# Kernel optimization log

Hardware: AMD Instinct MI355X
Metric: run time of the kernel (lower is better)

## Reference

```python
import jax, jax.numpy as jnp
import numpy as np

ALPHA = 0.01
EPS = ALPHA / (1.0 - 2.0 * ALPHA)  # boundary_eps


def setup_inputs() -> dict:
    key = jax.random.key(0)
    ks = jax.random.split(key, 9)
    B, D, K = 32768, 256, 1024
    x = jax.random.normal(ks[0], (B, D), dtype=jnp.float32)
    logp = jnp.zeros((B, 1), dtype=jnp.float32)
    actnorm1_bias = jax.random.normal(ks[1], (D,), dtype=jnp.float32) * 0.1
    actnorm1_weight = jax.random.normal(ks[2], (D,), dtype=jnp.float32) * 0.1
    actnorm2_bias = jax.random.normal(ks[3], (D,), dtype=jnp.float32) * 0.1
    actnorm2_weight = jax.random.normal(ks[4], (D,), dtype=jnp.float32) * 0.1
    shift_coeff = jax.random.normal(ks[5], (D,), dtype=jnp.float32)
    anchor_pts = jax.random.normal(ks[6], (K, D), dtype=jnp.float32)
    mixture_logits = jax.random.normal(ks[7], (K,), dtype=jnp.float32) * 0.1
    u = jax.random.uniform(ks[8], (D,), dtype=jnp.float32)
    box_min = -(u + 1.0) * 2.0  # guarantees box_max > box_min
    box_max = (u + 1.0) * 2.0
    return dict(x=x, logp=logp, actnorm1_bias=actnorm1_bias,
                actnorm1_weight=actnorm1_weight, actnorm2_bias=actnorm2_bias,
                actnorm2_weight=actnorm2_weight, shift_coeff=shift_coeff,
                anchor_pts=anchor_pts, mixture_logits=mixture_logits,
                box_min=box_min, box_max=box_max)


def _voronoi_forward(x, logp, a1b, a1w, a2b, a2w, shift_raw, anchors, mix_logits,
                     box_min, box_max):
    B, D = x.shape
    # actnorm1: y = (x + bias) * exp(weight); logp -= logdet
    x = (x + a1b) * jnp.exp(a1w)
    logp = logp - jnp.sum(a1w)
    # logit_transform.inverse: x = (sigmoid(x) - alpha) / (1 - 2*alpha)
    s = jax.nn.sigmoid(x)
    logdet = jnp.sum(jax.nn.log_sigmoid(x) + jax.nn.log_sigmoid(-x)
                     - jnp.log(1.0 - 2.0 * ALPHA), axis=1, keepdims=True)
    x = (s - ALPHA) / (1.0 - 2.0 * ALPHA)
    logp = logp - logdet
    # rescale from [-eps, 1+eps] to [0, 1]
    lo, hi = -EPS, 1.0 + EPS
    x = (x - lo) / (hi - lo)
    logp = logp - (-jnp.log(hi - lo) * D)
    # box constraints: affine to [box_min, box_max]
    x = x * (box_max - box_min) + box_min
    logp = logp - jnp.sum(jnp.log(box_max - box_min))
    # find_nearest: argmin squared distance over K anchors (GEMM form, no BxKxD tensor)
    d2 = (jnp.sum(x * x, axis=1, keepdims=True)
          - 2.0 * x @ anchors.T
          + jnp.sum(anchors * anchors, axis=1))  # [B, K]
    idx = jnp.argmin(d2, axis=1)  # [B]
    x_k = anchors[idx]  # gather nearest anchor, [B, D]
    # shift toward the nearest anchor
    sc = jax.nn.sigmoid(shift_raw) * 0.98 + 0.01  # (0.01, 0.99)
    x = x + sc * (x_k - x)
    logp = logp - jnp.sum(jnp.log(1.0 - sc))
    # map_outside_cell: identity with zero logdet (see notes)
    # recentre on the chosen anchor
    x = x - x_k
    # actnorm2
    x = (x + a2b) * jnp.exp(a2w)
    logp = logp - jnp.sum(a2w)
    # mixture log-prob gather
    logp_k = jax.nn.log_softmax(mix_logits)[idx][:, None]
    logp = logp - logp_k
    return x, logp, idx


def reference(x, logp, actnorm1_bias, actnorm1_weight, actnorm2_bias,
              actnorm2_weight, shift_coeff, anchor_pts, mixture_logits,
              box_min, box_max):
    return _voronoi_forward(x, logp, actnorm1_bias, actnorm1_weight,
                            actnorm2_bias, actnorm2_weight, shift_coeff,
                            anchor_pts, mixture_logits, box_min, box_max)
```

## Files before the change

### kernel.cpp

```cpp
#include <hip/hip_runtime.h>
#include <math.h>

namespace {
constexpr int Brows = 32768;
constexpr int Dd = 256;
constexpr int Kk = 1024;

constexpr double kAlpha64 = 0.01;
constexpr double kC164 = 1.0 - 2.0 * 0.01;
constexpr double kEps64 = 0.01 / (1.0 - 2.0 * 0.01);
constexpr double kLo64 = -kEps64;
constexpr double kHi64 = 1.0 + kEps64;

constexpr int WS_E1W = 0;
constexpr int WS_WD = 256;
constexpr int WS_P = 512;
constexpr int WS_Q = 768;
constexpr int WS_C = 1024;
constexpr int WS_AA = 1088;
constexpr int WS_LSM = 2112;
}

__global__ void precol_kernel(const float* __restrict__ a1w,
                              const float* __restrict__ a2w,
                              const float* __restrict__ a2b,
                              const float* __restrict__ shiftc,
                              const float* __restrict__ bmin,
                              const float* __restrict__ bmax,
                              float* __restrict__ ws) {
  const int d = threadIdx.x;
  const float w1 = a1w[d], w2 = a2w[d];
  const float wd = __fsub_rn(bmax[d], bmin[d]);
  const float sc = 1.0f / (1.0f + expf(-shiftc[d])) * 0.98f + 0.01f;
  const float e2 = expf(w2);
  ws[WS_E1W + d] = expf(w1);
  ws[WS_WD + d] = wd;
  ws[WS_P + d] = (1.0f - sc) * e2;
  ws[WS_Q + d] = a2b[d] * e2;
  float contrib = -w1 - w2 - logf(wd) - logf(1.0f - sc);
#pragma unroll
  for (int o = 32; o > 0; o >>= 1) contrib += __shfl_xor(contrib, o, 64);
  __shared__ float red[4];
  if ((d & 63) == 0) red[d >> 6] = contrib;
  __syncthreads();
  if (d == 0) {
    float Cv = red[0] + red[1] + red[2] + red[3];
    Cv += (float)Dd * (float)(log(kC164) + log(kHi64 - kLo64));
    ws[WS_C] = Cv;
  }
}

template <typename F>
__device__ inline float pw128_sq(F ld) {
  float r[8];
#pragma unroll
  for (int j = 0; j < 8; ++j) {
    const float v = ld(j);
    r[j] = __fmul_rn(v, v);
  }
  for (int i = 8; i < 128; i += 8) {
#pragma unroll
    for (int j = 0; j < 8; ++j) {
      const float v = ld(i + j);
      r[j] = __fadd_rn(r[j], __fmul_rn(v, v));
    }
  }
  const float s01 = __fadd_rn(r[0], r[1]);
  const float s23 = __fadd_rn(r[2], r[3]);
  const float s45 = __fadd_rn(r[4], r[5]);
  const float s67 = __fadd_rn(r[6], r[7]);
  return __fadd_rn(__fadd_rn(s01, s23), __fadd_rn(s45, s67));
}

__global__ void anorm_kernel(const float* __restrict__ anchors,
                             float* __restrict__ ws) {
  const int k = blockIdx.x * 256 + threadIdx.x;
  const float* a = anchors + (size_t)k * Dd;
  const float b0 = pw128_sq([&](int i) { return a[i]; });
  const float b1 = pw128_sq([&](int i) { return a[128 + i]; });
  ws[WS_AA + k] = __fadd_rn(b0, b1);
}

__global__ void lsm_kernel(const float* __restrict__ logits,
                           float* __restrict__ ws) {
  __shared__ float sm[1024];
  const int t = threadIdx.x;
  const float v = logits[t];
  sm[t] = v;
  __syncthreads();
  for (int o = 512; o > 0; o >>= 1) {
    if (t < o) sm[t] = fmaxf(sm[t], sm[t + o]);
    __syncthreads();
  }
  const float mx = sm[0];
  __syncthreads();
  sm[t] = expf(v - mx);
  __syncthreads();
  for (int o = 512; o > 0; o >>= 1) {
    if (t < o) sm[t] += sm[t + o];
    __syncthreads();
  }
  const float lse = mx + logf(sm[0]);
  ws[WS_LSM + t] = v - lse;
}

__global__ __launch_bounds__(256, 2) void voronoi_main(
    const float* __restrict__ x, const float* __restrict__ logp_in,
    const float* __restrict__ a1b, const float* __restrict__ anchors,
    const float* __restrict__ bmin, const float* __restrict__ ws,
    float* __restrict__ out) {
  __shared__ float xt[Dd][68];
  __shared__ float at[32][68];
  __shared__ float logdet_s[64];
  __shared__ float xx_s[64];
  __shared__ int bidx_s[64];

  const int t = threadIdx.x;
  const int r0 = blockIdx.x * 64;

  const float LOF = (float)kLo64;
  const float HLF = (float)(kHi64 - kLo64);
  const float ALPHAF = (float)kAlpha64;
  const float C1F = (float)kC164;

  {
    const int r = t >> 2, j = t & 3;
    const float* xrow = x + (size_t)(r0 + r) * Dd;
    float ld = 0.0f;
#pragma unroll
    for (int it = 0; it < 16; ++it) {
      const int c = it * 16 + j * 4;
      const float4 xv = *(const float4*)(xrow + c);
      const float4 bv = *(const float4*)(a1b + c);
      const float4 ev = *(const float4*)(ws + WS_E1W + c);
      const float4 wv = *(const float4*)(ws + WS_WD + c);
      const float4 mv = *(const float4*)(bmin + c);
      const float xs[4] = {xv.x, xv.y, xv.z, xv.w};
      const float bs[4] = {bv.x, bv.y, bv.z, bv.w};
      const float es[4] = {ev.x, ev.y, ev.z, ev.w};
      const float wds[4] = {wv.x, wv.y, wv.z, wv.w};
      const float ms[4] = {mv.x, mv.y, mv.z, mv.w};
#pragma unroll
      for (int w = 0; w < 4; ++w) {
        const float y = __fmul_rn(__fadd_rn(xs[w], bs[w]), es[w]);
        const float ay = fabsf(y);
        const float e = expf(-ay);
        ld += -ay - 2.0f * log1pf(e);
        const float den = __fadd_rn(1.0f, e);
        const float s =
            (y >= 0.0f) ? __fdiv_rn(1.0f, den) : __fdiv_rn(e, den);
        const float x3 = __fdiv_rn(__fsub_rn(s, ALPHAF), C1F);
        const float x4v = __fdiv_rn(__fsub_rn(x3, LOF), HLF);
        const float x5 = __fadd_rn(__fmul_rn(x4v, wds[w]), ms[w]);
        xt[c + w][r] = x5;
      }
    }
    ld += __shfl_xor(ld, 1, 64);
    ld += __shfl_xor(ld, 2, 64);
    if (j == 0) logdet_s[r] = ld;
  }
  __syncthreads();

  if (t < 64) {
    const float b0 = pw128_sq([&](int i) { return xt[i][t]; });
    const float b1 = pw128_sq([&](int i) { return xt[128 + i][t]; });
    xx_s[t] = __fadd_rn(b0, b1);
  }
  __syncthreads();

  const int tc = t & 15, tr = t >> 4;
  const int tr4 = tr * 4, tc4 = tc * 4;
  float xxr[4];
#pragma unroll
  for (int i = 0; i < 4; ++i) xxr[i] = xx_s[tr4 + i];
  float bd2[4];
  int bidx[4];
#pragma unroll
  for (int i = 0; i < 4; ++i) {
    bd2[i] = 3.0e38f;
    bidx[i] = 0;
  }

  for (int kt = 0; kt < 16; ++kt) {
    float acc[4][4];
#pragma unroll
    for (int i = 0; i < 4; ++i)
#pragma unroll
      for (int j = 0; j < 4; ++j) acc[i][j] = 0.0f;

    for (int dc = 0; dc < 8; ++dc) {
      __syncthreads();
#pragma unroll
      for (int m = 0; m < 2; ++m) {
        const int f = t + m * 256;
        const int kk = f >> 3, cp = f & 7;
        const float4 av = *(const float4*)(anchors +
                                           (size_t)(kt * 64 + kk) * Dd +
                                           dc * 32 + cp * 4);
        at[cp * 4 + 0][kk] = av.x;
        at[cp * 4 + 1][kk] = av.y;
        at[cp * 4 + 2][kk] = av.z;
        at[cp * 4 + 3][kk] = av.w;
      }
      __syncthreads();
      const int db = dc * 32;
#pragma unroll
      for (int dd = 0; dd < 32; ++dd) {
        const float4 xf = *(const float4*)(&xt[db + dd][tr4]);
        const float4 af = *(const float4*)(&at[dd][tc4]);
        acc[0][0] = fmaf(xf.x, af.x, acc[0][0]);
        acc[0][1] = fmaf(xf.x, af.y, acc[0][1]);
        acc[0][2] = fmaf(xf.x, af.z, acc[0][2]);
        acc[0][3] = fmaf(xf.x, af.w, acc[0][3]);
        acc[1][0] = fmaf(xf.y, af.x, acc[1][0]);
        acc[1][1] = fmaf(xf.y, af.y, acc[1][1]);
        acc[1][2] = fmaf(xf.y, af.z, acc[1][2]);
        acc[1][3] = fmaf(xf.y, af.w, acc[1][3]);
        acc[2][0] = fmaf(xf.z, af.x, acc[2][0]);
        acc[2][1] = fmaf(xf.z, af.y, acc[2][1]);
        acc[2][2] = fmaf(xf.z, af.z, acc[2][2]);
        acc[2][3] = fmaf(xf.z, af.w, acc[2][3]);
        acc[3][0] = fmaf(xf.w, af.x, acc[3][0]);
        acc[3][1] = fmaf(xf.w, af.y, acc[3][1]);
        acc[3][2] = fmaf(xf.w, af.z, acc[3][2]);
        acc[3][3] = fmaf(xf.w, af.w, acc[3][3]);
      }
    }
#pragma unroll
    for (int j = 0; j < 4; ++j) {
      const int k = kt * 64 + tc4 + j;
      const float aa = ws[WS_AA + k];
#pragma unroll
      for (int i = 0; i < 4; ++i) {
        const float twod = __fadd_rn(acc[i][j], acc[i][j]);
        const float d2 = __fadd_rn(__fsub_rn(xxr[i], twod), aa);
        if (d2 < bd2[i]) {
          bd2[i] = d2;
          bidx[i] = k;
        }
      }
    }
  }
#pragma unroll
  for (int o = 1; o < 16; o <<= 1) {
#pragma unroll
    for (int i = 0; i < 4; ++i) {
      const float od = __shfl_xor(bd2[i], o, 64);
      const int oi = __shfl_xor(bidx[i], o, 64);
      if (od < bd2[i] || (od == bd2[i] && oi < bidx[i])) {
        bd2[i] = od;
        bidx[i] = oi;
      }
    }
  }
  if (tc == 0) {
#pragma unroll
    for (int i = 0; i < 4; ++i) bidx_s[tr4 + i] = bidx[i];
  }
  __syncthreads();

  {
    const int r = t >> 2, j = t & 3;
    const int k = bidx_s[r];
    const float* arow = anchors + (size_t)k * Dd;
    float* orow = out + (size_t)(r0 + r) * Dd;
#pragma unroll
    for (int it = 0; it < 16; ++it) {
      const int c = it * 16 + j * 4;
      const float4 av = *(const float4*)(arow + c);
      const float4 pv = *(const float4*)(ws + WS_P + c);
      const float4 qv = *(const float4*)(ws + WS_Q + c);
      float4 ov;
      ov.x = fmaf(xt[c + 0][r] - av.x, pv.x, qv.x);
      ov.y = fmaf(xt[c + 1][r] - av.y, pv.y, qv.y);
      ov.z = fmaf(xt[c + 2][r] - av.z, pv.z, qv.z);
      ov.w = fmaf(xt[c + 3][r] - av.w, pv.w, qv.w);
      *(float4*)(orow + c) = ov;
    }
  }
  if (t < 64) {
    const int rr = t;
    const int kk2 = bidx_s[rr];
    const float lp =
        logp_in[r0 + rr] + ws[WS_C] - logdet_s[rr] - ws[WS_LSM + kk2];
    out[(size_t)Brows * Dd + r0 + rr] = lp;
    out[(size_t)Brows * Dd + Brows + r0 + rr] = (float)kk2;
  }
}

extern "C" void kernel_launch(void* const* d_in, const int* in_sizes, int n_in,
                              void* d_out, int out_size, void* d_ws,
                              size_t ws_size, hipStream_t stream) {
  const float* x = (const float*)d_in[0];
  const float* logp = (const float*)d_in[1];
  const float* a1b = (const float*)d_in[2];
  const float* a1w = (const float*)d_in[3];
  const float* a2b = (const float*)d_in[4];
  const float* a2w = (const float*)d_in[5];
  const float* shiftc = (const float*)d_in[6];
  const float* anch = (const float*)d_in[7];
  const float* mixl = (const float*)d_in[8];
  const float* bmin = (const float*)d_in[9];
  const float* bmax = (const float*)d_in[10];
  float* ws = (float*)d_ws;
  float* out = (float*)d_out;

  precol_kernel<<<1, 256, 0, stream>>>(a1w, a2w, a2b, shiftc, bmin, bmax, ws);
  anorm_kernel<<<Kk / 256, 256, 0, stream>>>(anch, ws);
  lsm_kernel<<<1, 1024, 0, stream>>>(mixl, ws);
  voronoi_main<<<Brows / 64, 256, 0, stream>>>(x, logp, a1b, anch, bmin, ws,
                                               out);
}
```

Baseline: 424.2 us.

## Enlarge per-thread register tile to 16x4 and widen anchor tile to 256

Measured after the change: 379.9 us. 1.12x faster.

```diff
diff --git a/kernel.cpp b/kernel.cpp
--- a/kernel.cpp
+++ b/kernel.cpp
@@ -110,7 +110,7 @@
     const float* __restrict__ bmin, const float* __restrict__ ws,
     float* __restrict__ out) {
   __shared__ float xt[Dd][68];
-  __shared__ float at[32][68];
+  __shared__ float at[8][256];
   __shared__ float logdet_s[64];
   __shared__ float xx_s[64];
   __shared__ int bidx_s[64];
@@ -147,8 +147,7 @@
         const float e = expf(-ay);
         ld += -ay - 2.0f * log1pf(e);
         const float den = __fadd_rn(1.0f, e);
-        const float s =
-            (y >= 0.0f) ? __fdiv_rn(1.0f, den) : __fdiv_rn(e, den);
+        const float s = (y >= 0.0f) ? __fdiv_rn(1.0f, den) : __fdiv_rn(e, den);
         const float x3 = __fdiv_rn(__fsub_rn(s, ALPHAF), C1F);
         const float x4v = __fdiv_rn(__fsub_rn(x3, LOF), HLF);
         const float x5 = __fadd_rn(__fmul_rn(x4v, wds[w]), ms[w]);
@@ -168,70 +167,70 @@
   }
   __syncthreads();
 
-  const int tc = t & 15, tr = t >> 4;
-  const int tr4 = tr * 4, tc4 = tc * 4;
-  float xxr[4];
-#pragma unroll
-  for (int i = 0; i < 4; ++i) xxr[i] = xx_s[tr4 + i];
-  float bd2[4];
-  int bidx[4];
-#pragma unroll
-  for (int i = 0; i < 4; ++i) {
+  const int tc = t & 63;
+  const int tr = t >> 6;
+  const int tr16 = tr * 16, tc4 = tc * 4;
+
+  float xxr[16];
+#pragma unroll
+  for (int i = 0; i < 16; ++i) xxr[i] = xx_s[tr16 + i];
+
+  float bd2[16];
+  int bidx[16];
+#pragma unroll
+  for (int i = 0; i < 16; ++i) {
     bd2[i] = 3.0e38f;
     bidx[i] = 0;
   }
 
-  for (int kt = 0; kt < 16; ++kt) {
-    float acc[4][4];
-#pragma unroll
-    for (int i = 0; i < 4; ++i)
+  for (int kt = 0; kt < 4; ++kt) {
+    float acc[16][4];
+#pragma unroll
+    for (int i = 0; i < 16; ++i)
 #pragma unroll
       for (int j = 0; j < 4; ++j) acc[i][j] = 0.0f;
 
-    for (int dc = 0; dc < 8; ++dc) {
+    for (int dc = 0; dc < 32; ++dc) {
       __syncthreads();
 #pragma unroll
       for (int m = 0; m < 2; ++m) {
-        const int f = t + m * 256;
-        const int kk = f >> 3, cp = f & 7;
+        const int u = t + m * 256;
+        const int k = u >> 1, q = u & 1;
         const float4 av = *(const float4*)(anchors +
-                                           (size_t)(kt * 64 + kk) * Dd +
-                                           dc * 32 + cp * 4);
-        at[cp * 4 + 0][kk] = av.x;
-        at[cp * 4 + 1][kk] = av.y;
-        at[cp * 4 + 2][kk] = av.z;
-        at[cp * 4 + 3][kk] = av.w;
+                                           (size_t)(kt * 256 + k) * Dd +
+                                           dc * 8 + q * 4);
+        at[q * 4 + 0][k] = av.x;
+        at[q * 4 + 1][k] = av.y;
+        at[q * 4 + 2][k] = av.z;
+        at[q * 4 + 3][k] = av.w;
       }
       __syncthreads();
-      const int db = dc * 32;
-#pragma unroll
-      for (int dd = 0; dd < 32; ++dd) {
-        const float4 xf = *(const float4*)(&xt[db + dd][tr4]);
+#pragma unroll
+      for (int dd = 0; dd < 8; ++dd) {
+        const int dg = dc * 8 + dd;
+        const float4 xf0 = *(const float4*)(&xt[dg][tr16]);
+        const float4 xf1 = *(const float4*)(&xt[dg][tr16 + 4]);
+        const float4 xf2 = *(const float4*)(&xt[dg][tr16 + 8]);
+        const float4 xf3 = *(const float4*)(&xt[dg][tr16 + 12]);
         const float4 af = *(const float4*)(&at[dd][tc4]);
-        acc[0][0] = fmaf(xf.x, af.x, acc[0][0]);
-        acc[0][1] = fmaf(xf.x, af.y, acc[0][1]);
-        acc[0][2] = fmaf(xf.x, af.z, acc[0][2]);
-        acc[0][3] = fmaf(xf.x, af.w, acc[0][3]);
-        acc[1][0] = fmaf(xf.y, af.x, acc[1][0]);
-        acc[1][1] = fmaf(xf.y, af.y, acc[1][1]);
-        acc[1][2] = fmaf(xf.y, af.z, acc[1][2]);
-        acc[1][3] = fmaf(xf.y, af.w, acc[1][3]);
-        acc[2][0] = fmaf(xf.z, af.x, acc[2][0]);
-        acc[2][1] = fmaf(xf.z, af.y, acc[2][1]);
-        acc[2][2] = fmaf(xf.z, af.z, acc[2][2]);
-        acc[2][3] = fmaf(xf.z, af.w, acc[2][3]);
-        acc[3][0] = fmaf(xf.w, af.x, acc[3][0]);
-        acc[3][1] = fmaf(xf.w, af.y, acc[3][1]);
-        acc[3][2] = fmaf(xf.w, af.z, acc[3][2]);
-        acc[3][3] = fmaf(xf.w, af.w, acc[3][3]);
+        const float xv[16] = {xf0.x, xf0.y, xf0.z, xf0.w, xf1.x, xf1.y,
+                              xf1.z, xf1.w, xf2.x, xf2.y, xf2.z, xf2.w,
+                              xf3.x, xf3.y, xf3.z, xf3.w};
+#pragma unroll
+        for (int i = 0; i < 16; ++i) {
+          acc[i][0] = fmaf(xv[i], af.x, acc[i][0]);
+          acc[i][1] = fmaf(xv[i], af.y, acc[i][1]);
+          acc[i][2] = fmaf(xv[i], af.z, acc[i][2]);
+          acc[i][3] = fmaf(xv[i], af.w, acc[i][3]);
+        }
       }
     }
 #pragma unroll
     for (int j = 0; j < 4; ++j) {
-      const int k = kt * 64 + tc4 + j;
+      const int k = kt * 256 + tc4 + j;
       const float aa = ws[WS_AA + k];
 #pragma unroll
-      for (int i = 0; i < 4; ++i) {
+      for (int i = 0; i < 16; ++i) {
         const float twod = __fadd_rn(acc[i][j], acc[i][j]);
         const float d2 = __fadd_rn(__fsub_rn(xxr[i], twod), aa);
         if (d2 < bd2[i]) {
@@ -242,9 +241,9 @@
     }
   }
 #pragma unroll
-  for (int o = 1; o < 16; o <<= 1) {
-#pragma unroll
-    for (int i = 0; i < 4; ++i) {
+  for (int o = 1; o < 64; o <<= 1) {
+#pragma unroll
+    for (int i = 0; i < 16; ++i) {
       const float od = __shfl_xor(bd2[i], o, 64);
       const int oi = __shfl_xor(bidx[i], o, 64);
       if (od < bd2[i] || (od == bd2[i] && oi < bidx[i])) {
@@ -255,7 +254,7 @@
   }
   if (tc == 0) {
 #pragma unroll
-    for (int i = 0; i < 4; ++i) bidx_s[tr4 + i] = bidx[i];
+    for (int i = 0; i < 16; ++i) bidx_s[tr16 + i] = bidx[i];
   }
   __syncthreads();
 
```
